# Optimization experiments

Hardware: AMD Instinct MI355X
Metric: run time of the kernel (lower is better)

Reference implementation:

```python
import jax, jax.numpy as jnp
import numpy as np

N_NODES = 100000
N_EDGES = 3200000
N_FEAT = 24
LAYERS = 6
VAL_SCALE = 0.01  # keep repeated SpMM numerically tame


def setup_inputs() -> dict:
    key = jax.random.key(0)
    k1, k2, k3, k4 = jax.random.split(key, 4)
    x = jax.random.normal(k1, (N_NODES, N_FEAT), dtype=jnp.float32)
    values = jax.random.normal(k2, (N_EDGES,), dtype=jnp.float32) * VAL_SCALE
    row_idx = jax.random.randint(k3, (N_EDGES,), 0, N_NODES, dtype=jnp.int64)
    col_idx = jax.random.randint(k4, (N_EDGES,), 0, N_NODES, dtype=jnp.int64)
    return {"x": x, "values": values, "row_idx": row_idx, "col_idx": col_idx}


def _spmm(values, row_idx, col_idx, x):
    # out[r] = sum_{e: row[e]==r} values[e] * x[col[e]]   (COO SpMM)
    msgs = values[:, None] * x[col_idx]  # [E, F] gather + scale
    return jax.ops.segment_sum(msgs, row_idx, num_segments=N_NODES)


def reference(x, values, row_idx, col_idx):
    # Faithful to AdultConnectome.forward: result = A^LAYERS @ x with fixed
    # COO sparsity (torch.sparse.mm applied layer_number times).
    result = x
    for _ in range(LAYERS):
        result = _spmm(values, row_idx, col_idx, result)
    return result
```

## Files before the change

kernel.cpp:

```cpp
#include <hip/hip_runtime.h>

#define N_NODES 100000
#define N_EDGES 3200000
#define N_FEAT 24
#define PADF4 8
#define BSHIFT 7
#define BROWS 128
#define NBUCK ((N_NODES + BROWS - 1) >> BSHIFT)
#define EPT 16
#define TILE (256 * EPT)
#define NTILES ((N_EDGES + TILE - 1) / TILE)
#define CAP 4608
#define DMAX 256
#define NKEY (BROWS * 16)


__global__ void zero_kernel(int* __restrict__ p, int n) {
    int i = blockIdx.x * blockDim.x + threadIdx.x;
    if (i < n) p[i] = 0;
}

__global__ __launch_bounds__(256) void bhist_kernel(const int* __restrict__ row,
                                                    int* __restrict__ bcnt) {
    __shared__ int h[NBUCK];
    for (int i = threadIdx.x; i < NBUCK; i += 256) h[i] = 0;
    __syncthreads();
    int stride = gridDim.x * blockDim.x;
    for (int i = blockIdx.x * blockDim.x + threadIdx.x; i < N_EDGES; i += stride)
        atomicAdd(&h[row[i] >> BSHIFT], 1);
    __syncthreads();
    for (int i = threadIdx.x; i < NBUCK; i += 256) {
        int c = h[i];
        if (c) atomicAdd(&bcnt[i], c);
    }
}

__global__ __launch_bounds__(1024) void bscan_kernel(const int* __restrict__ bcnt,
                                                     int* __restrict__ bbase,
                                                     int* __restrict__ bcursor) {
    __shared__ int part[1024];
    int tid = threadIdx.x;
    int v = (tid < NBUCK) ? bcnt[tid] : 0;
    part[tid] = v;
    __syncthreads();
    for (int off = 1; off < 1024; off <<= 1) {
        int p = (tid >= off) ? part[tid - off] : 0;
        __syncthreads();
        part[tid] += p;
        __syncthreads();
    }
    int ex = (tid > 0) ? part[tid - 1] : 0;
    if (tid <= NBUCK) {
        bbase[tid] = ex;
        if (tid < NBUCK) bcursor[tid] = ex;
    }
}

__global__ __launch_bounds__(256) void part_kernel(const int* __restrict__ row,
                                                   const int* __restrict__ col,
                                                   const float* __restrict__ val,
                                                   int* __restrict__ bcursor,
                                                   int2* __restrict__ epk) {
    __shared__ int h[NBUCK];
    __shared__ int lstart[NBUCK];
    __shared__ int delta[NBUCK];
    __shared__ int psum[256];
    __shared__ int2 stage[TILE];
    __shared__ unsigned short bidx[TILE];
    const int tid = threadIdx.x;
    for (int i = tid; i < NBUCK; i += 256) h[i] = 0;
    __syncthreads();

    const int tbase = blockIdx.x * TILE;
    const int m = min(TILE, N_EDGES - tbase);
    const int base = tbase + tid * EPT;
    int rowj[EPT], rk[EPT];
    #pragma unroll
    for (int j = 0; j < EPT; ++j) {
        int e = base + j;
        if (e < N_EDGES) {
            int r = row[e];
            rowj[j] = r;
            rk[j] = atomicAdd(&h[r >> BSHIFT], 1);
        } else rowj[j] = -1;
    }
    __syncthreads();

    {
        int lo = tid * 4;
        int hi = min(NBUCK, lo + 4);
        int s = 0;
        for (int j = lo; j < hi; ++j) s += h[j];
        psum[tid] = s;
        __syncthreads();
        for (int off = 1; off < 256; off <<= 1) {
            int p = (tid >= off) ? psum[tid - off] : 0;
            __syncthreads();
            psum[tid] += p;
            __syncthreads();
        }
        int run = (tid > 0) ? psum[tid - 1] : 0;
        for (int j = lo; j < hi; ++j) {
            lstart[j] = run;
            run += h[j];
        }
    }
    __syncthreads();

    for (int i = tid; i < NBUCK; i += 256) {
        int c = h[i];
        int g = c ? atomicAdd(&bcursor[i], c) : 0;
        delta[i] = g - lstart[i];
    }
    __syncthreads();

    #pragma unroll
    for (int j = 0; j < EPT; ++j) {
        if (rowj[j] >= 0) {
            int e = base + j;
            int b = rowj[j] >> BSHIFT;
            int rl = rowj[j] & (BROWS - 1);
            int slot = lstart[b] + rk[j];
            int2 pk;
            pk.x = col[e] | (rl << 17);
            pk.y = __float_as_int(val[e]);
            stage[slot] = pk;
            bidx[slot] = (unsigned short)b;
        }
    }
    __syncthreads();

    for (int i = tid; i < m; i += 256) {
        int b = bidx[i];
        epk[delta[b] + i] = stage[i];
    }
}

__global__ __launch_bounds__(256) void place_kernel(const int* __restrict__ bbase,
                                                    int2* __restrict__ epk,
                                                    int* __restrict__ starts,
                                                    int* __restrict__ dcnt) {
    __shared__ int kcnt[NKEY];
    __shared__ int kcur[NKEY];
    __shared__ int psum[256];
    __shared__ int dh[DMAX];
    __shared__ int2 stage[CAP];
    int b = blockIdx.x;
    int tid = threadIdx.x;
    int gb = bbase[b];
    int n = bbase[b + 1] - gb;
    for (int j = tid; j < NKEY; j += 256) kcnt[j] = 0;
    dh[tid] = 0;
    __syncthreads();
    for (int i = tid; i < n; i += 256) {
        int x = epk[gb + i].x;
        int key = (((x >> 17) & (BROWS - 1)) << 4) | ((x >> 13) & 15);
        atomicAdd(&kcnt[key], 1);
    }
    __syncthreads();
    int deg = 0;
    if (tid < BROWS) {
        int lo = tid << 4;
        #pragma unroll
        for (int j = 0; j < 16; ++j) deg += kcnt[lo + j];
    }
    int r_glob = (b << BSHIFT) + tid;
    if (tid < BROWS && r_glob < N_NODES) atomicAdd(&dh[min(deg, DMAX - 1)], 1);
    psum[tid] = deg;
    __syncthreads();
    for (int off = 1; off < 256; off <<= 1) {
        int p = (tid >= off) ? psum[tid - off] : 0;
        __syncthreads();
        psum[tid] += p;
        __syncthreads();
    }
    int run = (tid > 0) ? psum[tid - 1] : 0;
    if (tid < BROWS && r_glob < N_NODES) starts[r_glob] = gb + run;
    if (b == 0 && tid == 0) starts[N_NODES] = N_EDGES;
    if (tid < BROWS) {
        int lo = tid << 4;
        #pragma unroll
        for (int j = 0; j < 16; ++j) {
            kcur[lo + j] = run;
            run += kcnt[lo + j];
        }
    }
    __syncthreads();
    {
        int c = dh[tid];
        if (c) atomicAdd(&dcnt[tid], c);
    }
    for (int i = tid; i < n; i += 256) {
        int2 p = epk[gb + i];
        int key = (((p.x >> 17) & (BROWS - 1)) << 4) | ((p.x >> 13) & 15);
        int slot = atomicAdd(&kcur[key], 1);
        int2 fin;
        fin.x = p.x & 0x1FFFF;
        fin.y = p.y;
        if (slot < CAP) stage[slot] = fin;
        else epk[gb + slot] = fin;
    }
    __syncthreads();
    for (int i = tid; i < n && i < CAP; i += 256) epk[gb + i] = stage[i];
}

__global__ __launch_bounds__(256) void dscan_kernel(const int* __restrict__ dcnt,
                                                    int* __restrict__ dcur) {
    __shared__ int part[DMAX];
    int tid = threadIdx.x;
    int v = dcnt[tid];
    part[tid] = v;
    __syncthreads();
    for (int off = 1; off < DMAX; off <<= 1) {
        int p = (tid >= off) ? part[tid - off] : 0;
        __syncthreads();
        part[tid] += p;
        __syncthreads();
    }
    dcur[tid] = part[tid] - v;
}

__global__ __launch_bounds__(256) void dscatter_kernel(const int* __restrict__ starts,
                                                       int* __restrict__ dcur,
                                                       int* __restrict__ perm) {
    __shared__ int h[DMAX];
    __shared__ int chunk[DMAX];
    int tid = threadIdx.x;
    int r = blockIdx.x * 256 + tid;
    h[tid] = 0;
    __syncthreads();
    int d = -1, rk = 0;
    if (r < N_NODES) {
        d = min(starts[r + 1] - starts[r], DMAX - 1);
        rk = atomicAdd(&h[d], 1);
    }
    __syncthreads();
    int c = h[tid];
    chunk[tid] = c ? atomicAdd(&dcur[tid], c) : 0;
    __syncthreads();
    if (r < N_NODES) perm[chunk[d] + rk] = r;
}

__global__ __launch_bounds__(256) void pad_copy_kernel(const float4* __restrict__ x4,
                                                       float4* __restrict__ dst) {
    int t = blockIdx.x * blockDim.x + threadIdx.x;
    int r = t >> 3;
    if (r >= N_NODES) return;
    int sub = t & 7;
    float4 v;
    if (sub < 6) v = x4[r * 6 + sub];
    else         v = make_float4(0.f, 0.f, 0.f, 0.f);
    dst[r * PADF4 + sub] = v;
}

#define ACC4(v, xv, a)                                       \
    a.x = fmaf(v, xv.x, a.x); a.y = fmaf(v, xv.y, a.y);      \
    a.z = fmaf(v, xv.z, a.z); a.w = fmaf(v, xv.w, a.w);

__global__ __launch_bounds__(256) void spmm_pad_kernel(const int* __restrict__ starts,
                                                       const int* __restrict__ perm,
                                                       const int2* __restrict__ epk,
                                                       const float4* __restrict__ src,
                                                       float4* __restrict__ dst) {
    int t = blockIdx.x * blockDim.x + threadIdx.x;
    int g = t >> 3;
    if (g >= N_NODES) return;
    int rowi = perm[g];
    int sub = t & 7;
    int s = starts[rowi];
    int e = starts[rowi + 1];
    const float4* sp = src + sub;
    float4 acc = make_float4(0.f, 0.f, 0.f, 0.f);
    int i = s;
    for (; i + 3 < e; i += 4) {
        int2 p0 = epk[i];
        int2 p1 = epk[i + 1];
        int2 p2 = epk[i + 2];
        int2 p3 = epk[i + 3];
        float4 x0 = sp[p0.x * PADF4];
        float4 x1 = sp[p1.x * PADF4];
        float4 x2 = sp[p2.x * PADF4];
        float4 x3 = sp[p3.x * PADF4];
        float v0 = __int_as_float(p0.y);
        float v1 = __int_as_float(p1.y);
        float v2 = __int_as_float(p2.y);
        float v3 = __int_as_float(p3.y);
        ACC4(v0, x0, acc);
        ACC4(v1, x1, acc);
        ACC4(v2, x2, acc);
        ACC4(v3, x3, acc);
    }
    for (; i < e; ++i) {
        int2 p = epk[i];
        float4 xv = sp[p.x * PADF4];
        float v = __int_as_float(p.y);
        ACC4(v, xv, acc);
    }
    dst[rowi * PADF4 + sub] = acc;
}

__global__ __launch_bounds__(256) void spmm_final_kernel(const int* __restrict__ starts,
                                                         const int* __restrict__ perm,
                                                         const int2* __restrict__ epk,
                                                         const float4* __restrict__ src,
                                                         float* __restrict__ out) {
    int t = blockIdx.x * blockDim.x + threadIdx.x;
    int g = t >> 3;
    if (g >= N_NODES) return;
    int rowi = perm[g];
    int sub = t & 7;
    int s = starts[rowi];
    int e = starts[rowi + 1];
    const float4* sp = src + sub;
    float4 acc = make_float4(0.f, 0.f, 0.f, 0.f);
    int i = s;
    for (; i + 3 < e; i += 4) {
        int2 p0 = epk[i];
        int2 p1 = epk[i + 1];
        int2 p2 = epk[i + 2];
        int2 p3 = epk[i + 3];
        float4 x0 = sp[p0.x * PADF4];
        float4 x1 = sp[p1.x * PADF4];
        float4 x2 = sp[p2.x * PADF4];
        float4 x3 = sp[p3.x * PADF4];
        float v0 = __int_as_float(p0.y);
        float v1 = __int_as_float(p1.y);
        float v2 = __int_as_float(p2.y);
        float v3 = __int_as_float(p3.y);
        ACC4(v0, x0, acc);
        ACC4(v1, x1, acc);
        ACC4(v2, x2, acc);
        ACC4(v3, x3, acc);
    }
    for (; i < e; ++i) {
        int2 p = epk[i];
        float4 xv = sp[p.x * PADF4];
        float v = __int_as_float(p.y);
        ACC4(v, xv, acc);
    }
    if (sub < 6) *(float4*)(out + rowi * N_FEAT + sub * 4) = acc;
}


extern "C" void kernel_launch(void* const* d_in, const int* in_sizes, int n_in,
                              void* d_out, int out_size, void* d_ws, size_t ws_size,
                              hipStream_t stream) {
    const float* x       = (const float*)d_in[0];
    const float* values  = (const float*)d_in[1];
    const int*   row_idx = (const int*)d_in[2];
    const int*   col_idx = (const int*)d_in[3];
    float* out = (float*)d_out;

    char* ws = (char*)d_ws;
    int*    bcnt    = (int*)(ws + 0);
    int*    bbase   = (int*)(ws + 4096);
    int*    bcursor = (int*)(ws + 8192);
    int*    dcnt    = (int*)(ws + 12288);
    int*    dcur    = (int*)(ws + 16384);
    int*    starts  = (int*)(ws + 20480);
    int*    perm    = (int*)(ws + 420608);
    int2*   epk     = (int2*)(ws + 820736);
    float4* bufA    = (float4*)(ws + 26420864);
    float4* bufB    = (float4*)(ws + 39220864);

    zero_kernel<<<4, 256, 0, stream>>>(bcnt, NBUCK);
    zero_kernel<<<1, 256, 0, stream>>>(dcnt, DMAX);
    bhist_kernel<<<512, 256, 0, stream>>>(row_idx, bcnt);
    bscan_kernel<<<1, 1024, 0, stream>>>(bcnt, bbase, bcursor);
    part_kernel<<<NTILES, 256, 0, stream>>>(row_idx, col_idx, values, bcursor, epk);
    place_kernel<<<NBUCK, 256, 0, stream>>>(bbase, epk, starts, dcnt);

    const int node_blocks = (N_NODES + 255) / 256;
    dscan_kernel<<<1, DMAX, 0, stream>>>(dcnt, dcur);
    dscatter_kernel<<<node_blocks, 256, 0, stream>>>(starts, dcur, perm);

    const int spmm_blocks = (N_NODES * 8 + 255) / 256;
    pad_copy_kernel<<<spmm_blocks, 256, 0, stream>>>((const float4*)x, bufA);
    spmm_pad_kernel<<<spmm_blocks, 256, 0, stream>>>(starts, perm, epk, bufA, bufB);
    spmm_pad_kernel<<<spmm_blocks, 256, 0, stream>>>(starts, perm, epk, bufB, bufA);
    spmm_pad_kernel<<<spmm_blocks, 256, 0, stream>>>(starts, perm, epk, bufA, bufB);
    spmm_pad_kernel<<<spmm_blocks, 256, 0, stream>>>(starts, perm, epk, bufB, bufA);
    spmm_pad_kernel<<<spmm_blocks, 256, 0, stream>>>(starts, perm, epk, bufA, bufB);
    spmm_final_kernel<<<spmm_blocks, 256, 0, stream>>>(starts, perm, epk, bufB, out);
}
```

Baseline: 454.3 us.

## Unroll SpMM gather loop by 8, halve partition tile size, use memset for zeroing

Adds an 8-way unrolled edge loop ahead of the existing 4-way loop in the row-wise SpMM, so more independent gathers are in flight per thread and memory latency is better hidden. It also halves edges per thread in the partition kernel, which doubles the number of tiles, and replaces the two small zeroing kernels with hipMemsetAsync. The SpMM pad and final kernels now share one templated body. The risks are higher register pressure from the larger unroll and more partition blocks contending on the bucket cursors.

```diff
diff --git a/kernel.cpp b/kernel.cpp
--- a/kernel.cpp
+++ b/kernel.cpp
@@ -7,18 +7,12 @@
 #define BSHIFT 7
 #define BROWS 128
 #define NBUCK ((N_NODES + BROWS - 1) >> BSHIFT)
-#define EPT 16
+#define EPT 8
 #define TILE (256 * EPT)
 #define NTILES ((N_EDGES + TILE - 1) / TILE)
 #define CAP 4608
 #define DMAX 256
 #define NKEY (BROWS * 16)
-
-
-__global__ void zero_kernel(int* __restrict__ p, int n) {
-    int i = blockIdx.x * blockDim.x + threadIdx.x;
-    if (i < n) p[i] = 0;
-}
 
 __global__ __launch_bounds__(256) void bhist_kernel(const int* __restrict__ row,
                                                     int* __restrict__ bcnt) {
@@ -257,11 +251,13 @@
     a.x = fmaf(v, xv.x, a.x); a.y = fmaf(v, xv.y, a.y);      \
     a.z = fmaf(v, xv.z, a.z); a.w = fmaf(v, xv.w, a.w);
 
-__global__ __launch_bounds__(256) void spmm_pad_kernel(const int* __restrict__ starts,
-                                                       const int* __restrict__ perm,
-                                                       const int2* __restrict__ epk,
-                                                       const float4* __restrict__ src,
-                                                       float4* __restrict__ dst) {
+template <bool FINAL>
+__device__ __forceinline__ void spmm_body(const int* __restrict__ starts,
+                                          const int* __restrict__ perm,
+                                          const int2* __restrict__ epk,
+                                          const float4* __restrict__ src,
+                                          float4* __restrict__ dstp,
+                                          float* __restrict__ dstf) {
     int t = blockIdx.x * blockDim.x + threadIdx.x;
     int g = t >> 3;
     if (g >= N_NODES) return;
@@ -272,6 +268,32 @@
     const float4* sp = src + sub;
     float4 acc = make_float4(0.f, 0.f, 0.f, 0.f);
     int i = s;
+    for (; i + 7 < e; i += 8) {
+        int2 p0 = epk[i];
+        int2 p1 = epk[i + 1];
+        int2 p2 = epk[i + 2];
+        int2 p3 = epk[i + 3];
+        int2 p4 = epk[i + 4];
+        int2 p5 = epk[i + 5];
+        int2 p6 = epk[i + 6];
+        int2 p7 = epk[i + 7];
+        float4 x0 = sp[p0.x * PADF4];
+        float4 x1 = sp[p1.x * PADF4];
+        float4 x2 = sp[p2.x * PADF4];
+        float4 x3 = sp[p3.x * PADF4];
+        float4 x4 = sp[p4.x * PADF4];
+        float4 x5 = sp[p5.x * PADF4];
+        float4 x6 = sp[p6.x * PADF4];
+        float4 x7 = sp[p7.x * PADF4];
+        ACC4(__int_as_float(p0.y), x0, acc);
+        ACC4(__int_as_float(p1.y), x1, acc);
+        ACC4(__int_as_float(p2.y), x2, acc);
+        ACC4(__int_as_float(p3.y), x3, acc);
+        ACC4(__int_as_float(p4.y), x4, acc);
+        ACC4(__int_as_float(p5.y), x5, acc);
+        ACC4(__int_as_float(p6.y), x6, acc);
+        ACC4(__int_as_float(p7.y), x7, acc);
+    }
     for (; i + 3 < e; i += 4) {
         int2 p0 = epk[i];
         int2 p1 = epk[i + 1];
@@ -281,22 +303,29 @@
         float4 x1 = sp[p1.x * PADF4];
         float4 x2 = sp[p2.x * PADF4];
         float4 x3 = sp[p3.x * PADF4];
-        float v0 = __int_as_float(p0.y);
-        float v1 = __int_as_float(p1.y);
-        float v2 = __int_as_float(p2.y);
-        float v3 = __int_as_float(p3.y);
-        ACC4(v0, x0, acc);
-        ACC4(v1, x1, acc);
-        ACC4(v2, x2, acc);
-        ACC4(v3, x3, acc);
+        ACC4(__int_as_float(p0.y), x0, acc);
+        ACC4(__int_as_float(p1.y), x1, acc);
+        ACC4(__int_as_float(p2.y), x2, acc);
+        ACC4(__int_as_float(p3.y), x3, acc);
     }
     for (; i < e; ++i) {
         int2 p = epk[i];
         float4 xv = sp[p.x * PADF4];
-        float v = __int_as_float(p.y);
-        ACC4(v, xv, acc);
-    }
-    dst[rowi * PADF4 + sub] = acc;
+        ACC4(__int_as_float(p.y), xv, acc);
+    }
+    if (FINAL) {
+        if (sub < 6) *(float4*)(dstf + rowi * N_FEAT + sub * 4) = acc;
+    } else {
+        dstp[rowi * PADF4 + sub] = acc;
+    }
+}
+
+__global__ __launch_bounds__(256) void spmm_pad_kernel(const int* __restrict__ starts,
+                                                       const int* __restrict__ perm,
+                                                       const int2* __restrict__ epk,
+                                                       const float4* __restrict__ src,
+                                                       float4* __restrict__ dst) {
+    spmm_body<false>(starts, perm, epk, src, dst, nullptr);
 }
 
 __global__ __launch_bounds__(256) void spmm_final_kernel(const int* __restrict__ starts,
@@ -304,41 +333,7 @@
                                                          const int2* __restrict__ epk,
                                                          const float4* __restrict__ src,
                                                          float* __restrict__ out) {
-    int t = blockIdx.x * blockDim.x + threadIdx.x;
-    int g = t >> 3;
-    if (g >= N_NODES) return;
-    int rowi = perm[g];
-    int sub = t & 7;
-    int s = starts[rowi];
-    int e = starts[rowi + 1];
-    const float4* sp = src + sub;
-    float4 acc = make_float4(0.f, 0.f, 0.f, 0.f);
-    int i = s;
-    for (; i + 3 < e; i += 4) {
-        int2 p0 = epk[i];
-        int2 p1 = epk[i + 1];
-        int2 p2 = epk[i + 2];
-        int2 p3 = epk[i + 3];
-        float4 x0 = sp[p0.x * PADF4];
-        float4 x1 = sp[p1.x * PADF4];
-        float4 x2 = sp[p2.x * PADF4];
-        float4 x3 = sp[p3.x * PADF4];
-        float v0 = __int_as_float(p0.y);
-        float v1 = __int_as_float(p1.y);
-        float v2 = __int_as_float(p2.y);
-        float v3 = __int_as_float(p3.y);
-        ACC4(v0, x0, acc);
-        ACC4(v1, x1, acc);
-        ACC4(v2, x2, acc);
-        ACC4(v3, x3, acc);
-    }
-    for (; i < e; ++i) {
-        int2 p = epk[i];
-        float4 xv = sp[p.x * PADF4];
-        float v = __int_as_float(p.y);
-        ACC4(v, xv, acc);
-    }
-    if (sub < 6) *(float4*)(out + rowi * N_FEAT + sub * 4) = acc;
+    spmm_body<true>(starts, perm, epk, src, nullptr, out);
 }
 
 
@@ -363,8 +358,8 @@
     float4* bufA    = (float4*)(ws + 26420864);
     float4* bufB    = (float4*)(ws + 39220864);
 
-    zero_kernel<<<4, 256, 0, stream>>>(bcnt, NBUCK);
-    zero_kernel<<<1, 256, 0, stream>>>(dcnt, DMAX);
+    hipMemsetAsync(bcnt, 0, NBUCK * sizeof(int), stream);
+    hipMemsetAsync(dcnt, 0, DMAX * sizeof(int), stream);
     bhist_kernel<<<512, 256, 0, stream>>>(row_idx, bcnt);
     bscan_kernel<<<1, 1024, 0, stream>>>(bcnt, bbase, bcursor);
     part_kernel<<<NTILES, 256, 0, stream>>>(row_idx, col_idx, values, bcursor, epk);
```

Result: slower. 469.9 us (+3.4%).
